# Kernel optimization log

Measured on AMD Instinct MI355X. Metric: run time of the kernel, lower is better.

Reference implementation:

```python
import jax, jax.numpy as jnp
import numpy as np

HEADS = 4
LN_EPS = 1e-5

def layernorm(x, w, b):
    m = x.mean(-1, keepdims=True)
    v = ((x - m) ** 2).mean(-1, keepdims=True)
    return (x - m) * jax.lax.rsqrt(v + LN_EPS) * w + b

def conv3d(x, w, b, pad, dil=1, groups=1):
    out = jax.lax.conv_general_dilated(
        x, w, (1, 1, 1), [(pad, pad)] * 3,
        rhs_dilation=(dil, dil, dil),
        dimension_numbers=('NCDHW', 'OIDHW', 'NCDHW'),
        feature_group_count=groups)
    return out + b[None, :, None, None, None]

def trilinear_gather(x_flat, pz, py, px, D, H, W):
    # x_flat: [B,C,S]; pz/py/px: [B,S] fractional sample coords, zero padding outside
    z0f, y0f, x0f = jnp.floor(pz), jnp.floor(py), jnp.floor(px)
    wz, wy, wx = pz - z0f, py - y0f, px - x0f
    z0, y0, x0 = z0f.astype(jnp.int32), y0f.astype(jnp.int32), x0f.astype(jnp.int32)
    acc = jnp.zeros_like(x_flat)
    for dz in (0, 1):
        for dy in (0, 1):
            for dx in (0, 1):
                iz, iy, ix = z0 + dz, y0 + dy, x0 + dx
                cw = (wz if dz else 1.0 - wz) * (wy if dy else 1.0 - wy) * (wx if dx else 1.0 - wx)
                valid = (iz >= 0) & (iz < D) & (iy >= 0) & (iy < H) & (ix >= 0) & (ix < W)
                idx = (jnp.clip(iz, 0, D - 1) * H + jnp.clip(iy, 0, H - 1)) * W + jnp.clip(ix, 0, W - 1)
                vals = jnp.take_along_axis(x_flat, idx[:, None, :], axis=2)
                acc = acc + vals * (cw * valid)[:, None, :]
    return acc

def deform_conv3d(x, off_w, off_b, w, b):
    # DeformConvPack: offsets from a regular 3x3x3 conv, then offset trilinear sampling + conv
    B, C, D, H, W = x.shape
    K = 27
    offsets = conv3d(x, off_w, off_b, 1).reshape(B, K, 3, D * H * W)
    gz, gy, gx = jnp.indices((D, H, W))
    bz = gz.reshape(-1).astype(x.dtype)[None]
    by = gy.reshape(-1).astype(x.dtype)[None]
    bx = gx.reshape(-1).astype(x.dtype)[None]
    x_flat = x.reshape(B, C, -1)
    O = w.shape[0]
    wk = w.reshape(O, C, K)
    out = jnp.zeros((B, O, D * H * W), x.dtype)
    for k in range(K):  # fixed 27 kernel taps
        kz, ky, kx = k // 9, (k // 3) % 3, k % 3
        pz = bz + (kz - 1) + offsets[:, k, 0]
        py = by + (ky - 1) + offsets[:, k, 1]
        px = bx + (kx - 1) + offsets[:, k, 2]
        samp = trilinear_gather(x_flat, pz, py, px, D, H, W)  # [B,C,S]
        out = out + jnp.einsum('bcs,oc->bos', samp, wk[:, :, k])
    out = out + b[None, :, None]
    return out.reshape(B, O, D, H, W)

def forward(x, temperature, qkv_w, norm_w, norm_b, proj1_w, proj1_b, conv0_w, conv0_b,
            convsp_w, convsp_b, off_w, off_b, dcn_w, dcn_b, conv1_w, conv1_b,
            proj2_w, proj2_b, norm2_w, norm2_b, out_w, out_b, H, W, D):
    B, N, C = x.shape
    hd = C // HEADS
    qkv = (x @ qkv_w.T).reshape(B, N, 3, HEADS, hd).transpose(2, 0, 3, 1, 4)  # [3,B,h,N,hd]
    q = qkv[0].transpose(0, 1, 3, 2)  # [B,h,hd,N]
    k = qkv[1].transpose(0, 1, 3, 2)
    v = qkv[2].transpose(0, 1, 3, 2)
    q = q / jnp.maximum(jnp.sqrt((q * q).sum(-1, keepdims=True)), 1e-12)
    k = k / jnp.maximum(jnp.sqrt((k * k).sum(-1, keepdims=True)), 1e-12)
    attn = jnp.einsum('bhcn,bhdn->bhcd', q, k) * temperature[None]
    attn = jax.nn.softmax(attn, axis=-1)
    x_ca = jnp.einsum('bhcd,bhdn->bhcn', attn, v).transpose(0, 3, 1, 2).reshape(B, N, C)
    x_ca = layernorm(x_ca, norm_w, norm_b)
    x5 = x_ca.transpose(0, 2, 1).reshape(B, C, H, W, D)
    shortcut = x5
    y = jnp.einsum('bcxyz,oc->boxyz', x5, proj1_w) + proj1_b[None, :, None, None, None]
    y = jax.nn.gelu(y, approximate=False)
    u = y
    a = conv3d(y, conv0_w, conv0_b, 2, 1, C)      # depthwise k=5 pad=2
    a = conv3d(a, convsp_w, convsp_b, 9, 3, C)    # depthwise k=7 pad=9 dil=3
    a = deform_conv3d(a, off_w, off_b, dcn_w, dcn_b)
    a = jnp.einsum('bcxyz,oc->boxyz', a, conv1_w) + conv1_b[None, :, None, None, None]
    y = u * a
    y = jnp.einsum('bcxyz,oc->boxyz', y, proj2_w) + proj2_b[None, :, None, None, None]
    y = y + shortcut
    x_sa = y.reshape(B, C, N).transpose(0, 2, 1)           # lka returns [B,N,C]
    x_sa = x_sa.reshape(B, C, N).transpose(0, 2, 1)        # faithful torch reshape-after-permute
    x_sa = layernorm(x_sa, norm2_w, norm2_b)
    return x_sa @ out_w.T + out_b

def setup_inputs():
    key = jax.random.key(0)
    ks = jax.random.split(key, 12)
    B, C, H, W, D = 2, 64, 32, 32, 32
    N = H * W * D
    s = 0.02
    return dict(
        x=jax.random.normal(ks[0], (B, N, C), jnp.float32),
        temperature=jnp.ones((HEADS, 1, 1), jnp.float32),
        qkv_w=jax.random.normal(ks[1], (3 * C, C), jnp.float32) * s,
        norm_w=jnp.ones((C,), jnp.float32), norm_b=jnp.zeros((C,), jnp.float32),
        proj1_w=jax.random.normal(ks[2], (C, C), jnp.float32) * s,
        proj1_b=jnp.zeros((C,), jnp.float32),
        conv0_w=jax.random.normal(ks[3], (C, 1, 5, 5, 5), jnp.float32) * s,
        conv0_b=jnp.zeros((C,), jnp.float32),
        convsp_w=jax.random.normal(ks[4], (C, 1, 7, 7, 7), jnp.float32) * s,
        convsp_b=jnp.zeros((C,), jnp.float32),
        off_w=jax.random.normal(ks[5], (81, C, 3, 3, 3), jnp.float32) * 0.01,
        off_b=jnp.zeros((81,), jnp.float32),
        dcn_w=jax.random.normal(ks[6], (C, C, 3, 3, 3), jnp.float32) * s,
        dcn_b=jnp.zeros((C,), jnp.float32),
        conv1_w=jax.random.normal(ks[7], (C, C), jnp.float32) * s,
        conv1_b=jnp.zeros((C,), jnp.float32),
        proj2_w=jax.random.normal(ks[8], (C, C), jnp.float32) * s,
        proj2_b=jnp.zeros((C,), jnp.float32),
        norm2_w=jnp.ones((C,), jnp.float32), norm2_b=jnp.zeros((C,), jnp.float32),
        out_w=jax.random.normal(ks[9], (C, C), jnp.float32) * s,
        out_b=jnp.zeros((C,), jnp.float32),
        B_in=B, C_in=C, H=H, W=W, D=D,
    )

def reference(x, temperature, qkv_w, norm_w, norm_b, proj1_w, proj1_b, conv0_w, conv0_b,
              convsp_w, convsp_b, off_w, off_b, dcn_w, dcn_b, conv1_w, conv1_b,
              proj2_w, proj2_b, norm2_w, norm2_b, out_w, out_b, B_in, C_in, H, W, D):
    return forward(x, temperature, qkv_w, norm_w, norm_b, proj1_w, proj1_b, conv0_w, conv0_b,
                   convsp_w, convsp_b, off_w, off_b, dcn_w, dcn_b, conv1_w, conv1_b,
                   proj2_w, proj2_b, norm2_w, norm2_b, out_w, out_b, H, W, D)
```

## Files before the change

### kernel.cpp

```cpp
#include <hip/hip_runtime.h>
#include <hip/hip_bf16.h>

#define S 32768
#define BUFN (2*64*32768)

typedef __bf16 v8bf __attribute__((ext_vector_type(8)));
typedef float v4f __attribute__((ext_vector_type(4)));
typedef int v4i __attribute__((ext_vector_type(4)));

__device__ __forceinline__ ushort f2b(float f) {
  union { float f; unsigned u; } v; v.f = f;
  unsigned r = (v.u + 0x7fffu + ((v.u >> 16) & 1u)) >> 16;
  return (ushort)r;
}
__device__ __forceinline__ float b2f(ushort h) {
  union { unsigned u; float f; } v; v.u = ((unsigned)h) << 16;
  return v.f;
}
__device__ __forceinline__ float u2f(unsigned u) {
  union { unsigned u; float f; } v; v.u = u;
  return v.f;
}

__global__ void k_wt(const float* __restrict__ offw, const float* __restrict__ dcnw,
                     ushort* __restrict__ wt_off16, ushort* __restrict__ wt_dcn16) {
  int i = blockIdx.x*256 + threadIdx.x;
  if (i < 27*96*64) {
    int c = i & 63, o = (i >> 6) % 96, t = i / 6144;
    wt_off16[i] = (o < 81) ? f2b(offw[o*1728 + c*27 + t]) : (ushort)0;
  }
  if (i < 27*64*64) {
    int c = i & 63, o = (i >> 6) & 63, k = i >> 12;
    wt_dcn16[i] = f2b(dcnw[(o*64 + c)*27 + k]);
  }
}

__global__ __launch_bounds__(256) void k_qkv(const float* __restrict__ x,
    const float* __restrict__ qkv_w, float* __restrict__ q,
    float* __restrict__ k, float* __restrict__ v) {
  __shared__ float wsm[96*64];
  int half = blockIdx.x >> 8;
  int gid  = ((blockIdx.x & 255) << 8) + threadIdx.x;
  int rbase = half * 96;
  for (int i = threadIdx.x; i < 96*64; i += 256) wsm[i] = qkv_w[rbase*64 + i];
  __syncthreads();
  int b = gid >> 15, n = gid & (S-1);
  const float* xr = x + (size_t)gid * 64;
  float xv[64];
#pragma unroll
  for (int i = 0; i < 16; i++) {
    float4 t = ((const float4*)xr)[i];
    xv[4*i]=t.x; xv[4*i+1]=t.y; xv[4*i+2]=t.z; xv[4*i+3]=t.w;
  }
  for (int r = 0; r < 96; r++) {
    const float4* wr4 = (const float4*)&wsm[r*64];
    float acc = 0.f;
#pragma unroll
    for (int c4 = 0; c4 < 16; c4++) {
      float4 wv4 = wr4[c4];
      acc += xv[4*c4]*wv4.x + xv[4*c4+1]*wv4.y + xv[4*c4+2]*wv4.z + xv[4*c4+3]*wv4.w;
    }
    int row = rbase + r;
    float* dst = (row < 64) ? q : (row < 128 ? k : v);
    int ch = row & 63;
    dst[((size_t)(b*64 + ch))*S + n] = acc;
  }
}

__global__ __launch_bounds__(256) void k_rownorm(const float* __restrict__ q,
    const float* __restrict__ k, float* __restrict__ inv) {
  int row = blockIdx.x;
  const float* p = (row < 128) ? (q + (size_t)row*S) : (k + (size_t)(row-128)*S);
  const float4* p4 = (const float4*)p;
  float ss = 0.f;
  for (int i = threadIdx.x; i < S/4; i += 256) {
    float4 t = p4[i];
    ss += t.x*t.x + t.y*t.y + t.z*t.z + t.w*t.w;
  }
  __shared__ float red[256];
  red[threadIdx.x] = ss; __syncthreads();
  for (int st = 128; st > 0; st >>= 1) {
    if (threadIdx.x < st) red[threadIdx.x] += red[threadIdx.x+st];
    __syncthreads();
  }
  if (threadIdx.x == 0) inv[row] = 1.0f / fmaxf(sqrtf(red[0]), 1e-12f);
}

__global__ __launch_bounds__(256) void k_gram(const float* __restrict__ q,
    const float* __restrict__ k, float* __restrict__ gram) {
  __shared__ float qt[16][65], kt[16][65];
  int bi = blockIdx.x;
  int b = bi >> 7, h = (bi >> 5) & 3, chunk = bi & 31;
  int c = threadIdx.x >> 4, d = threadIdx.x & 15;
  const float* qb = q + ((size_t)(b*64 + h*16))*S;
  const float* kb = k + ((size_t)(b*64 + h*16))*S;
  int lr = threadIdx.x >> 4, lc = (threadIdx.x & 15) * 4;
  float acc = 0.f;
  for (int n0 = chunk*1024; n0 < chunk*1024 + 1024; n0 += 64) {
    float4 tq = *(const float4*)(qb + (size_t)lr*S + n0 + lc);
    float4 tk = *(const float4*)(kb + (size_t)lr*S + n0 + lc);
    __syncthreads();
    qt[lr][lc]=tq.x; qt[lr][lc+1]=tq.y; qt[lr][lc+2]=tq.z; qt[lr][lc+3]=tq.w;
    kt[lr][lc]=tk.x; kt[lr][lc+1]=tk.y; kt[lr][lc+2]=tk.z; kt[lr][lc+3]=tk.w;
    __syncthreads();
#pragma unroll
    for (int nn = 0; nn < 64; nn++) acc += qt[c][nn]*kt[d][nn];
  }
  atomicAdd(&gram[((b*4+h)*16+c)*16 + d], acc);
}

__global__ __launch_bounds__(256) void k_xca_ln(const float* __restrict__ v,
    const float* __restrict__ gram, const float* __restrict__ inv,
    const float* __restrict__ temp,
    const float* __restrict__ nw, const float* __restrict__ nb,
    float* __restrict__ x5) {
  __shared__ float at[1024];
  __shared__ float wsh[64], bsh[64];
  int gid = blockIdx.x*256 + threadIdx.x;
  int b = gid >> 15, n = gid & (S-1);
  int tid = threadIdx.x;
  if (tid < 64) {
    int h = tid >> 4, c = tid & 15;
    float iq = inv[b*64 + h*16 + c];
    float tp = temp[h];
    float l[16], m = -1e30f;
#pragma unroll
    for (int d = 0; d < 16; d++) {
      float vv = gram[((b*4+h)*16+c)*16 + d] * iq * inv[128 + b*64 + h*16 + d] * tp;
      l[d] = vv; m = fmaxf(m, vv);
    }
    float s = 0.f;
#pragma unroll
    for (int d = 0; d < 16; d++) { l[d] = expf(l[d]-m); s += l[d]; }
    float is = 1.0f / s;
#pragma unroll
    for (int d = 0; d < 16; d++) at[(h*16+c)*16 + d] = l[d]*is;
  } else if (tid < 128) {
    wsh[tid-64] = nw[tid-64]; bsh[tid-64] = nb[tid-64];
  }
  __syncthreads();
  const float* vb = v + (size_t)b*64*S + n;
  float vv[64];
#pragma unroll
  for (int ch = 0; ch < 64; ch++) vv[ch] = vb[(size_t)ch*S];
  float xc[64];
#pragma unroll
  for (int h = 0; h < 4; h++)
#pragma unroll
    for (int cc = 0; cc < 16; cc++) {
      float a = 0.f;
#pragma unroll
      for (int d = 0; d < 16; d++) a += at[(h*16+cc)*16 + d] * vv[h*16+d];
      xc[h*16+cc] = a;
    }
  float mean = 0.f;
#pragma unroll
  for (int ch = 0; ch < 64; ch++) mean += xc[ch];
  mean *= (1.0f/64.0f);
  float var = 0.f;
#pragma unroll
  for (int ch = 0; ch < 64; ch++) { float d = xc[ch]-mean; var += d*d; }
  var *= (1.0f/64.0f);
  float rs = rsqrtf(var + 1e-5f);
  float* xb = x5 + (size_t)b*64*S + n;
#pragma unroll
  for (int ch = 0; ch < 64; ch++)
    xb[(size_t)ch*S] = (xc[ch]-mean)*rs*wsh[ch] + bsh[ch];
}

__global__ __launch_bounds__(256) void k_proj1(const float* __restrict__ x5,
    const float* __restrict__ w, const float* __restrict__ bias, float* __restrict__ u) {
  __shared__ float wsm[32*64];
  __shared__ float bsm[32];
  int half = blockIdx.x >> 8;
  int gid = ((blockIdx.x & 255) << 8) + threadIdx.x;
  int o0 = half*32;
  for (int i = threadIdx.x; i < 32*64; i += 256) wsm[i] = w[o0*64 + i];
  if (threadIdx.x < 32) bsm[threadIdx.x] = bias[o0 + threadIdx.x];
  __syncthreads();
  int b = gid >> 15, n = gid & (S-1);
  const float* xb = x5 + (size_t)b*64*S + n;
  float xv[64];
#pragma unroll
  for (int ch = 0; ch < 64; ch++) xv[ch] = xb[(size_t)ch*S];
  float* ub = u + (size_t)b*64*S + n;
  for (int oo = 0; oo < 32; oo++) {
    const float4* wr4 = (const float4*)&wsm[oo*64];
    float acc = bsm[oo];
#pragma unroll
    for (int c4 = 0; c4 < 16; c4++) {
      float4 wv4 = wr4[c4];
      acc += xv[4*c4]*wv4.x + xv[4*c4+1]*wv4.y + xv[4*c4+2]*wv4.z + xv[4*c4+3]*wv4.w;
    }
    float g = 0.5f*acc*(1.0f + erff(acc*0.70710678118654752f));
    ub[(size_t)(o0+oo)*S] = g;
  }
}

__global__ __launch_bounds__(256) void k_conv0(const float* __restrict__ in,
    const float* __restrict__ w, const float* __restrict__ bias, ushort* __restrict__ out) {
  __shared__ ushort tile[5*32*40];
  __shared__ float wsh[128];
  int bi = blockIdx.x;
  int z = bi & 31, c = (bi >> 5) & 63, b = bi >> 11;
  const float* ib = in + ((size_t)(b*64+c) << 15);
  for (int i = threadIdx.x; i < 800; i += 256)
    ((int4*)tile)[i] = make_int4(0,0,0,0);
  if (threadIdx.x < 125) wsh[threadIdx.x] = w[c*125 + threadIdx.x];
  __syncthreads();
  for (int i = threadIdx.x; i < 5*1024; i += 256) {
    int dz = i >> 10, r = i & 1023;
    int zg = z + dz - 2;
    if (zg >= 0 && zg < 32)
      tile[(dz*32 + (r >> 5))*40 + (r & 31) + 2] = f2b(ib[zg*1024 + r]);
  }
  __syncthreads();
  int y = threadIdx.x >> 3, x0 = (threadIdx.x & 7) << 2;
  float bv = bias[c];
  float acc[4] = {bv, bv, bv, bv};
  for (int dz = 0; dz < 5; dz++) {
#pragma unroll
    for (int dy = 0; dy < 5; dy++) {
      int yy = y + dy - 2;
      if (yy < 0 || yy >= 32) continue;
      const float* wp = &wsh[(dz*5+dy)*5];
      float wreg[5];
#pragma unroll
      for (int dx = 0; dx < 5; dx++) wreg[dx] = wp[dx];
      const ushort* rp = &tile[(dz*32+yy)*40 + x0];
      int2 rl = *(const int2*)rp;
      int2 rh = *(const int2*)(rp + 4);
      float row[8];
      row[0]=u2f(((unsigned)rl.x)<<16); row[1]=u2f(rl.x & 0xffff0000u);
      row[2]=u2f(((unsigned)rl.y)<<16); row[3]=u2f(rl.y & 0xffff0000u);
      row[4]=u2f(((unsigned)rh.x)<<16); row[5]=u2f(rh.x & 0xffff0000u);
      row[6]=u2f(((unsigned)rh.y)<<16); row[7]=u2f(rh.y & 0xffff0000u);
#pragma unroll
      for (int dx = 0; dx < 5; dx++)
#pragma unroll
        for (int j = 0; j < 4; j++)
          acc[j] += wreg[dx] * row[dx+j];
    }
  }
  ushort* ob = out + ((size_t)(b*64+c) << 15) + z*1024 + y*32 + x0;
  unsigned p0 = (unsigned)f2b(acc[0]) | ((unsigned)f2b(acc[1]) << 16);
  unsigned p1 = (unsigned)f2b(acc[2]) | ((unsigned)f2b(acc[3]) << 16);
  *(int2*)ob = make_int2((int)p0, (int)p1);
}

__global__ __launch_bounds__(256) void k_convsp(const ushort* __restrict__ in,
    const float* __restrict__ w, const float* __restrict__ bias, ushort* __restrict__ out) {
  __shared__ ushort tile[7*32*56];
  __shared__ float wsh[344];
  int bi = blockIdx.x;
  int z = bi & 31, c = (bi >> 5) & 63, b = bi >> 11;
  const ushort* ib = in + ((size_t)(b*64+c) << 15);
  for (int i = threadIdx.x; i < 1568; i += 256)
    ((int4*)tile)[i] = make_int4(0,0,0,0);
  for (int i = threadIdx.x; i < 343; i += 256) wsh[i] = w[c*343 + i];
  __syncthreads();
  for (int i = threadIdx.x; i < 7*1024; i += 256) {
    int t = i >> 10, r = i & 1023;
    int zg = z + 3*t - 9;
    if (zg >= 0 && zg < 32)
      tile[(t*32 + (r >> 5))*56 + (r & 31) + 9] = ib[zg*1024 + r];
  }
  __syncthreads();
  int y = threadIdx.x >> 3, x0 = (threadIdx.x & 7) << 2;
  float bv = bias[c];
  float acc[4] = {bv, bv, bv, bv};
  for (int t = 0; t < 7; t++) {
#pragma unroll
    for (int dy = 0; dy < 7; dy++) {
      int yy = y + 3*dy - 9;
      if (yy < 0 || yy >= 32) continue;
      const float* wp = &wsh[(t*7+dy)*7];
      float wreg[7];
#pragma unroll
      for (int dx = 0; dx < 7; dx++) wreg[dx] = wp[dx];
      const ushort* rp = &tile[(t*32+yy)*56 + x0];
      float row[24];
#pragma unroll
      for (int qq = 0; qq < 6; qq++) {
        int2 rv = *(const int2*)(rp + 4*qq);
        row[4*qq+0]=u2f(((unsigned)rv.x)<<16); row[4*qq+1]=u2f(rv.x & 0xffff0000u);
        row[4*qq+2]=u2f(((unsigned)rv.y)<<16); row[4*qq+3]=u2f(rv.y & 0xffff0000u);
      }
#pragma unroll
      for (int dx = 0; dx < 7; dx++)
#pragma unroll
        for (int j = 0; j < 4; j++)
          acc[j] += wreg[dx] * row[3*dx+j];
    }
  }
  ushort* ob = out + ((size_t)(b*64+c) << 15) + z*1024 + y*32 + x0;
  unsigned p0 = (unsigned)f2b(acc[0]) | ((unsigned)f2b(acc[1]) << 16);
  unsigned p1 = (unsigned)f2b(acc[2]) | ((unsigned)f2b(acc[3]) << 16);
  *(int2*)ob = make_int2((int)p0, (int)p1);
}

__global__ __launch_bounds__(256) void k_tr(const ushort* __restrict__ a2,
                                            ushort* __restrict__ a2t) {
  __shared__ ushort tile[64*66];
  int bi = blockIdx.x;
  int b = bi >> 9, chunk = bi & 511;
  int s0 = chunk << 6;
  const ushort* ib = a2 + ((size_t)b << 21) + s0;
#pragma unroll
  for (int i = 0; i < 16; i++) {
    int j = threadIdx.x + (i << 8);
    int c = j >> 6, sl = j & 63;
    tile[c*66 + sl] = ib[((size_t)c << 15) + sl];
  }
  __syncthreads();
  ushort* ob = a2t + ((size_t)b << 21) + ((size_t)s0 << 6);
#pragma unroll
  for (int i = 0; i < 16; i++) {
    int j = threadIdx.x + (i << 8);
    int sl = j >> 6, c = j & 63;
    ob[sl*64 + c] = tile[c*66 + sl];
  }
}

__global__ __launch_bounds__(256) void k_offconv(const ushort* __restrict__ a2t,
    const ushort* __restrict__ wt16, float* __restrict__ off) {
  int bi = blockIdx.x;
  int b = bi >> 9, tile = bi & 511;
  int s0 = tile << 6;
  int tid = threadIdx.x;
  int lane = tid & 63, wv = tid >> 6;
  int si = lane & 15, rq = lane >> 4, q8 = rq << 3;
  int sw = s0 + (wv << 4);
  int s_c = sw + si;
  int zc = s_c >> 10, yc = (s_c >> 5) & 31, xc = s_c & 31;
  const ushort* a2b = a2t + ((size_t)b << 21);
  v4f acc[6];
#pragma unroll
  for (int i = 0; i < 6; i++) acc[i] = (v4f){0.f,0.f,0.f,0.f};
  const v4i z4 = {0,0,0,0};
  for (int t = 0; t < 27; t++) {
    int kz = t/9, ky = (t/3)%3, kx = t%3;
    int zz = zc + kz - 1, yy = yc + ky - 1, xx = xc + kx - 1;
    bool ok = (zz>=0 && zz<32 && yy>=0 && yy<32 && xx>=0 && xx<32);
    v8bf b0 = __builtin_bit_cast(v8bf, z4);
    v8bf b1 = __builtin_bit_cast(v8bf, z4);
    if (ok) {
      const ushort* p = a2b + ((size_t)((zz<<10)+(yy<<5)+xx) << 6) + q8;
      b0 = *(const v8bf*)p;
      b1 = *(const v8bf*)(p + 32);
    }
    const ushort* wk = wt16 + t*6144;
#pragma unroll
    for (int ot = 0; ot < 6; ot++) {
      const ushort* ap = wk + (((ot<<4) + si) << 6) + q8;
      v8bf a0 = *(const v8bf*)ap;
      v8bf a1 = *(const v8bf*)(ap + 32);
      acc[ot] = __builtin_amdgcn_mfma_f32_16x16x32_bf16(a0, b0, acc[ot], 0,0,0);
      acc[ot] = __builtin_amdgcn_mfma_f32_16x16x32_bf16(a1, b1, acc[ot], 0,0,0);
    }
  }
#pragma unroll
  for (int ot = 0; ot < 6; ot++)
#pragma unroll
    for (int r = 0; r < 4; r++) {
      int o = ot*16 + rq*4 + r;
      if (o < 81)
        off[(((size_t)(b*81 + o)) << 15) + sw + si] = acc[ot][r];
    }
}

__global__ __launch_bounds__(256) void k_dcn(const ushort* __restrict__ a2t,
    const float* __restrict__ off, const float* __restrict__ off_b,
    const ushort* __restrict__ wt16, float* __restrict__ out) {
  __shared__ float ofs[81*66];
  __shared__ ushort scr[4][16*72];
  int bi = blockIdx.x;
  int b = bi >> 9, tile = bi & 511;
  int s0 = tile << 6;
  int tid = threadIdx.x;
  const float* offbase = off + (((size_t)(b*81)) << 15) + s0;
  for (int i = tid; i < 5184; i += 256) {
    int r = i >> 6, sl = i & 63;
    ofs[r*66 + sl] = offbase[((size_t)r << 15) + sl] + off_b[r];
  }
  __syncthreads();
  int lane = tid & 63, wv = tid >> 6;
  int sr = lane >> 3, cs = lane & 7;
  int si = lane & 15, rq = lane >> 4;
  int sw = s0 + (wv << 4);
  const ushort* a2b = a2t + ((size_t)b << 21);
  ushort* myscr = &scr[wv][0];
  int sA = sw + sr, sB = sw + 8 + sr;
  int zA = sA >> 10, yA = (sA >> 5) & 31, xA = sA & 31;
  int zB = sB >> 10, yB = (sB >> 5) & 31, xB = sB & 31;
  int slcA = (wv << 4) + sr, slcB = slcA + 8;
  v4f acc[4];
#pragma unroll
  for (int t = 0; t < 4; t++) acc[t] = (v4f){0.f,0.f,0.f,0.f};
  for (int k = 0; k < 27; k++) {
    int kz = k/9, ky = (k/3)%3, kx = k%3;
    int idxA[8], idxB[8];
    float wA[8], wB[8];
    {
      float pz = (float)(zA + kz - 1) + ofs[(3*k+0)*66 + slcA];
      float py = (float)(yA + ky - 1) + ofs[(3*k+1)*66 + slcA];
      float px = (float)(xA + kx - 1) + ofs[(3*k+2)*66 + slcA];
      float fz = floorf(pz), fy = floorf(py), fx = floorf(px);
      float wz = pz-fz, wy = py-fy, wx = px-fx;
      int z0 = (int)fz, y0 = (int)fy, x0 = (int)fx;
      int zi[2], yi[2], xi[2]; float zw[2], yw[2], xw[2];
#pragma unroll
      for (int d = 0; d < 2; d++) {
        int iz = z0 + d; zi[d] = min(max(iz,0),31) << 10;
        zw[d] = (iz >= 0 && iz < 32) ? (d ? wz : 1.f-wz) : 0.f;
        int iy = y0 + d; yi[d] = min(max(iy,0),31) << 5;
        yw[d] = (iy >= 0 && iy < 32) ? (d ? wy : 1.f-wy) : 0.f;
        int ix = x0 + d; xi[d] = min(max(ix,0),31);
        xw[d] = (ix >= 0 && ix < 32) ? (d ? wx : 1.f-wx) : 0.f;
      }
#pragma unroll
      for (int r = 0; r < 8; r++) {
        int dz = r >> 2, dy = (r >> 1) & 1, dx = r & 1;
        idxA[r] = zi[dz] + yi[dy] + xi[dx];
        wA[r] = zw[dz] * yw[dy] * xw[dx];
      }
    }
    {
      float pz = (float)(zB + kz - 1) + ofs[(3*k+0)*66 + slcB];
      float py = (float)(yB + ky - 1) + ofs[(3*k+1)*66 + slcB];
      float px = (float)(xB + kx - 1) + ofs[(3*k+2)*66 + slcB];
      float fz = floorf(pz), fy = floorf(py), fx = floorf(px);
      float wz = pz-fz, wy = py-fy, wx = px-fx;
      int z0 = (int)fz, y0 = (int)fy, x0 = (int)fx;
      int zi[2], yi[2], xi[2]; float zw[2], yw[2], xw[2];
#pragma unroll
      for (int d = 0; d < 2; d++) {
        int iz = z0 + d; zi[d] = min(max(iz,0),31) << 10;
        zw[d] = (iz >= 0 && iz < 32) ? (d ? wz : 1.f-wz) : 0.f;
        int iy = y0 + d; yi[d] = min(max(iy,0),31) << 5;
        yw[d] = (iy >= 0 && iy < 32) ? (d ? wy : 1.f-wy) : 0.f;
        int ix = x0 + d; xi[d] = min(max(ix,0),31);
        xw[d] = (ix >= 0 && ix < 32) ? (d ? wx : 1.f-wx) : 0.f;
      }
#pragma unroll
      for (int r = 0; r < 8; r++) {
        int dz = r >> 2, dy = (r >> 1) & 1, dx = r & 1;
        idxB[r] = zi[dz] + yi[dy] + xi[dx];
        wB[r] = zw[dz] * yw[dy] * xw[dx];
      }
    }
    v4i gA[8], gB[8];
#pragma unroll
    for (int r = 0; r < 8; r++)
      gA[r] = *(const v4i*)(a2b + ((size_t)idxA[r] << 6) + (cs << 3));
#pragma unroll
    for (int r = 0; r < 8; r++)
      gB[r] = *(const v4i*)(a2b + ((size_t)idxB[r] << 6) + (cs << 3));
    float faA[8], faB[8];
#pragma unroll
    for (int j = 0; j < 8; j++) { faA[j] = 0.f; faB[j] = 0.f; }
#pragma unroll
    for (int r = 0; r < 8; r++) {
      float wa = wA[r], wb = wB[r];
#pragma unroll
      for (int m = 0; m < 4; m++) {
        unsigned da = (unsigned)gA[r][m];
        faA[2*m]   += wa * u2f(da << 16);
        faA[2*m+1] += wa * u2f(da & 0xffff0000u);
        unsigned db = (unsigned)gB[r][m];
        faB[2*m]   += wb * u2f(db << 16);
        faB[2*m+1] += wb * u2f(db & 0xffff0000u);
      }
    }
    v4i dA, dB;
#pragma unroll
    for (int m = 0; m < 4; m++) {
      unsigned l0 = (__float_as_uint(faA[2*m])   + 0x8000u) >> 16;
      unsigned h0 = (__float_as_uint(faA[2*m+1]) + 0x8000u) & 0xffff0000u;
      dA[m] = (int)(l0 | h0);
      unsigned l1 = (__float_as_uint(faB[2*m])   + 0x8000u) >> 16;
      unsigned h1 = (__float_as_uint(faB[2*m+1]) + 0x8000u) & 0xffff0000u;
      dB[m] = (int)(l1 | h1);
    }
    *(v4i*)&myscr[sr*72 + (cs << 3)]       = dA;
    *(v4i*)&myscr[(8+sr)*72 + (cs << 3)]   = dB;
    v8bf bf0 = *(const v8bf*)&myscr[si*72 + (rq << 3)];
    v8bf bf1 = *(const v8bf*)&myscr[si*72 + 32 + (rq << 3)];
    const ushort* wk = wt16 + (k << 12);
#pragma unroll
    for (int ot = 0; ot < 4; ot++) {
      const ushort* ap = wk + (((ot<<4) + si) << 6) + (rq << 3);
      v8bf a0 = *(const v8bf*)ap;
      v8bf a1 = *(const v8bf*)(ap + 32);
      acc[ot] = __builtin_amdgcn_mfma_f32_16x16x32_bf16(a0, bf0, acc[ot], 0,0,0);
      acc[ot] = __builtin_amdgcn_mfma_f32_16x16x32_bf16(a1, bf1, acc[ot], 0,0,0);
    }
  }
#pragma unroll
  for (int ot = 0; ot < 4; ot++)
#pragma unroll
    for (int r = 0; r < 4; r++) {
      int o = (ot << 4) + rq*4 + r;
      out[(((size_t)(b*64 + o)) << 15) + sw + si] = acc[ot][r];
    }
}

__global__ __launch_bounds__(256) void k_fuse2(const float* __restrict__ dcn0,
    const float* __restrict__ dcn_b, const float* __restrict__ c1w,
    const float* __restrict__ c1b, const float* __restrict__ u,
    const float* __restrict__ p2w, const float* __restrict__ p2b,
    const float* __restrict__ x5, float* __restrict__ y2) {
  __shared__ float w1[4096], w2[4096];
  __shared__ float b1[64], b2[64], db[64];
  int gid = blockIdx.x*256 + threadIdx.x;
  for (int i = threadIdx.x; i < 4096; i += 256) { w1[i] = c1w[i]; w2[i] = p2w[i]; }
  if (threadIdx.x < 64) {
    b1[threadIdx.x]=c1b[threadIdx.x]; b2[threadIdx.x]=p2b[threadIdx.x];
    db[threadIdx.x]=dcn_b[threadIdx.x];
  }
  __syncthreads();
  int b = gid >> 15, n = gid & (S-1);
  const float* dbp0 = dcn0 + (size_t)b*64*S + n;
  float dv[64];
#pragma unroll
  for (int c = 0; c < 64; c++)
    dv[c] = dbp0[(size_t)c*S] + db[c];
  const float* ub = u + (size_t)b*64*S + n;
  float m[64];
  for (int o = 0; o < 64; o++) {
    const float4* w4 = (const float4*)&w1[o*64];
    float a = b1[o];
#pragma unroll
    for (int c4 = 0; c4 < 16; c4++) {
      float4 wv4 = w4[c4];
      a += dv[4*c4]*wv4.x + dv[4*c4+1]*wv4.y + dv[4*c4+2]*wv4.z + dv[4*c4+3]*wv4.w;
    }
    m[o] = ub[(size_t)o*S] * a;
  }
  const float* sb = x5 + (size_t)b*64*S + n;
  float* yb = y2 + (size_t)b*64*S + n;
  for (int o = 0; o < 64; o++) {
    const float4* w4 = (const float4*)&w2[o*64];
    float a = b2[o];
#pragma unroll
    for (int c4 = 0; c4 < 16; c4++) {
      float4 wv4 = w4[c4];
      a += m[4*c4]*wv4.x + m[4*c4+1]*wv4.y + m[4*c4+2]*wv4.z + m[4*c4+3]*wv4.w;
    }
    yb[(size_t)o*S] = a + sb[(size_t)o*S];
  }
}

__global__ __launch_bounds__(256) void k_final(const float* __restrict__ y2,
    const float* __restrict__ n2w, const float* __restrict__ n2b,
    const float* __restrict__ ow, const float* __restrict__ ob, float* __restrict__ out) {
  __shared__ float wsh[4096];
  __shared__ float nw[64], nb[64], obs[64];
  int bi = blockIdx.x;
  int b = bi >> 7; int mg = (bi >> 4) & 7; int r0 = (bi & 15)*4;
  for (int i = threadIdx.x; i < 4096; i += 256) wsh[i] = ow[i];
  if (threadIdx.x < 64) {
    nw[threadIdx.x]=n2w[threadIdx.x]; nb[threadIdx.x]=n2b[threadIdx.x];
    obs[threadIdx.x]=ob[threadIdx.x];
  }
  __syncthreads();
  int mi = threadIdx.x & 63, rg = threadIdx.x >> 6;
  int r = r0 + rg;
  int m = mg*64 + mi;
  int n = m*64 + r;
  const float* yb = y2 + ((size_t)(b*64+r))*S + m;
  float v[64];
#pragma unroll
  for (int c = 0; c < 64; c++) v[c] = yb[(size_t)c*512];
  float mean = 0.f;
#pragma unroll
  for (int c = 0; c < 64; c++) mean += v[c];
  mean *= (1.0f/64.0f);
  float var = 0.f;
#pragma unroll
  for (int c = 0; c < 64; c++) { float d = v[c]-mean; var += d*d; }
  var *= (1.0f/64.0f);
  float rs = rsqrtf(var + 1e-5f);
#pragma unroll
  for (int c = 0; c < 64; c++) v[c] = (v[c]-mean)*rs*nw[c] + nb[c];
  float* orow = out + ((size_t)b*S + n)*64;
  for (int o4 = 0; o4 < 16; o4++) {
    const float4* w0 = (const float4*)&wsh[(o4*4+0)*64];
    const float4* w1 = (const float4*)&wsh[(o4*4+1)*64];
    const float4* w2 = (const float4*)&wsh[(o4*4+2)*64];
    const float4* w3 = (const float4*)&wsh[(o4*4+3)*64];
    float t0=obs[o4*4+0], t1=obs[o4*4+1], t2=obs[o4*4+2], t3=obs[o4*4+3];
#pragma unroll
    for (int c4 = 0; c4 < 16; c4++) {
      float4 a0 = w0[c4], a1 = w1[c4], a2 = w2[c4], a3 = w3[c4];
      float v0 = v[4*c4], v1 = v[4*c4+1], v2 = v[4*c4+2], v3 = v[4*c4+3];
      t0 += a0.x*v0 + a0.y*v1 + a0.z*v2 + a0.w*v3;
      t1 += a1.x*v0 + a1.y*v1 + a1.z*v2 + a1.w*v3;
      t2 += a2.x*v0 + a2.y*v1 + a2.z*v2 + a2.w*v3;
      t3 += a3.x*v0 + a3.y*v1 + a3.z*v2 + a3.w*v3;
    }
    float4 a; a.x=t0; a.y=t1; a.z=t2; a.w=t3;
    ((float4*)orow)[o4] = a;
  }
}

extern "C" void kernel_launch(void* const* d_in, const int* in_sizes, int n_in,
                              void* d_out, int out_size, void* d_ws, size_t ws_size,
                              hipStream_t stream) {
  const float* x      = (const float*)d_in[0];
  const float* temp   = (const float*)d_in[1];
  const float* qkv_w  = (const float*)d_in[2];
  const float* norm_w = (const float*)d_in[3];
  const float* norm_b = (const float*)d_in[4];
  const float* p1w    = (const float*)d_in[5];
  const float* p1b    = (const float*)d_in[6];
  const float* c0w    = (const float*)d_in[7];
  const float* c0b    = (const float*)d_in[8];
  const float* cspw   = (const float*)d_in[9];
  const float* cspb   = (const float*)d_in[10];
  const float* offw   = (const float*)d_in[11];
  const float* offb   = (const float*)d_in[12];
  const float* dcnw   = (const float*)d_in[13];
  const float* dcnb   = (const float*)d_in[14];
  const float* c1w    = (const float*)d_in[15];
  const float* c1b    = (const float*)d_in[16];
  const float* p2w    = (const float*)d_in[17];
  const float* p2b    = (const float*)d_in[18];
  const float* n2w    = (const float*)d_in[19];
  const float* n2b    = (const float*)d_in[20];
  const float* outw   = (const float*)d_in[21];
  const float* outb   = (const float*)d_in[22];
  float* out = (float*)d_out;

  float* Wa  = (float*)d_ws;
  float* Wb  = Wa + BUFN;
  float* Wc  = Wb + BUFN;
  float* OFF = Wc + BUFN;
  float* SM  = OFF + (size_t)2*81*S;
  float* SM_inv  = SM;
  float* SM_gram = SM + 256;
  ushort* WT_OFF16 = (ushort*)(SM + 4352);
  ushort* WT_DCN16 = WT_OFF16 + 165888;
  float* vbuf = out;
  ushort* A1_16 = (ushort*)d_out;
  ushort* A2_16 = (ushort*)Wc;
  ushort* a2t = (ushort*)d_out;

  hipMemsetAsync(SM, 0, 4352*sizeof(float), stream);
  k_wt     <<<648, 256, 0, stream>>>(offw, dcnw, WT_OFF16, WT_DCN16);

  k_qkv    <<<512, 256, 0, stream>>>(x, qkv_w, Wa, Wb, vbuf);
  k_rownorm<<<256, 256, 0, stream>>>(Wa, Wb, SM_inv);
  k_gram   <<<256, 256, 0, stream>>>(Wa, Wb, SM_gram);
  k_xca_ln <<<256, 256, 0, stream>>>(vbuf, SM_gram, SM_inv, temp, norm_w, norm_b, Wa);
  k_proj1  <<<512, 256, 0, stream>>>(Wa, p1w, p1b, Wb);
  k_conv0  <<<4096,256, 0, stream>>>(Wb, c0w, c0b, A1_16);
  k_convsp <<<4096,256, 0, stream>>>(A1_16, cspw, cspb, A2_16);
  k_tr     <<<1024,256, 0, stream>>>(A2_16, a2t);
  k_offconv<<<1024,256, 0, stream>>>(a2t, WT_OFF16, OFF);
  k_dcn    <<<1024,256, 0, stream>>>(a2t, OFF, offb, WT_DCN16, Wc);
  k_fuse2  <<<256, 256, 0, stream>>>(Wc, dcnb, c1w, c1b, Wb, p2w, p2b, Wa, OFF);
  k_final  <<<256, 256, 0, stream>>>(OFF, n2w, n2b, outw, outb, out);
}
```

Baseline: 833.7 us.

## Use bf16 MFMA for QKV and proj1 pointwise projections

Rewrites the QKV and proj1 1x1 projections to use 16x16x32 bf16 MFMA instructions instead of scalar fp32 FMA loops. Weights are pre-converted to bf16 in the weight-prep kernel, and activations are converted to bf16 in registers before the matrix ops. This is meant to cut the ALU-bound per-thread dot products and the LDS weight staging, at the cost of bf16 rounding of inputs and weights in these two projections.

```diff
diff --git a/kernel.cpp b/kernel.cpp
--- a/kernel.cpp
+++ b/kernel.cpp
@@ -23,7 +23,9 @@
 }
 
 __global__ void k_wt(const float* __restrict__ offw, const float* __restrict__ dcnw,
-                     ushort* __restrict__ wt_off16, ushort* __restrict__ wt_dcn16) {
+                     const float* __restrict__ qkvw, const float* __restrict__ p1w,
+                     ushort* __restrict__ wt_off16, ushort* __restrict__ wt_dcn16,
+                     ushort* __restrict__ qkv16, ushort* __restrict__ p1w16) {
   int i = blockIdx.x*256 + threadIdx.x;
   if (i < 27*96*64) {
     int c = i & 63, o = (i >> 6) % 96, t = i / 6144;
@@ -33,37 +35,54 @@
     int c = i & 63, o = (i >> 6) & 63, k = i >> 12;
     wt_dcn16[i] = f2b(dcnw[(o*64 + c)*27 + k]);
   }
+  if (i < 12288) qkv16[i] = f2b(qkvw[i]);
+  if (i < 4096)  p1w16[i] = f2b(p1w[i]);
 }
 
 __global__ __launch_bounds__(256) void k_qkv(const float* __restrict__ x,
-    const float* __restrict__ qkv_w, float* __restrict__ q,
+    const ushort* __restrict__ qkvw16, float* __restrict__ q,
     float* __restrict__ k, float* __restrict__ v) {
-  __shared__ float wsm[96*64];
-  int half = blockIdx.x >> 8;
-  int gid  = ((blockIdx.x & 255) << 8) + threadIdx.x;
-  int rbase = half * 96;
-  for (int i = threadIdx.x; i < 96*64; i += 256) wsm[i] = qkv_w[rbase*64 + i];
-  __syncthreads();
-  int b = gid >> 15, n = gid & (S-1);
-  const float* xr = x + (size_t)gid * 64;
-  float xv[64];
-#pragma unroll
-  for (int i = 0; i < 16; i++) {
-    float4 t = ((const float4*)xr)[i];
-    xv[4*i]=t.x; xv[4*i+1]=t.y; xv[4*i+2]=t.z; xv[4*i+3]=t.w;
-  }
-  for (int r = 0; r < 96; r++) {
-    const float4* wr4 = (const float4*)&wsm[r*64];
-    float acc = 0.f;
-#pragma unroll
-    for (int c4 = 0; c4 < 16; c4++) {
-      float4 wv4 = wr4[c4];
-      acc += xv[4*c4]*wv4.x + xv[4*c4+1]*wv4.y + xv[4*c4+2]*wv4.z + xv[4*c4+3]*wv4.w;
-    }
-    int row = rbase + r;
-    float* dst = (row < 64) ? q : (row < 128 ? k : v);
-    int ch = row & 63;
-    dst[((size_t)(b*64 + ch))*S + n] = acc;
+  int bi = blockIdx.x;
+  int b = bi >> 9, tile = bi & 511;
+  int tid = threadIdx.x;
+  int lane = tid & 63, wv = tid >> 6;
+  int si = lane & 15, rq = lane >> 4, q8 = rq << 3;
+  int s = (tile << 6) + (wv << 4) + si;
+  const float* xr = x + ((size_t)(b*S + s) << 6);
+  float4 t0 = *(const float4*)(xr + q8);
+  float4 t1 = *(const float4*)(xr + q8 + 4);
+  float4 t2 = *(const float4*)(xr + q8 + 32);
+  float4 t3 = *(const float4*)(xr + q8 + 36);
+  float f0[8] = {t0.x,t0.y,t0.z,t0.w,t1.x,t1.y,t1.z,t1.w};
+  float f1[8] = {t2.x,t2.y,t2.z,t2.w,t3.x,t3.y,t3.z,t3.w};
+  v4i d0, d1;
+#pragma unroll
+  for (int m = 0; m < 4; m++) {
+    d0[m] = (int)((unsigned)f2b(f0[2*m]) | ((unsigned)f2b(f0[2*m+1]) << 16));
+    d1[m] = (int)((unsigned)f2b(f1[2*m]) | ((unsigned)f2b(f1[2*m+1]) << 16));
+  }
+  v8bf b0 = __builtin_bit_cast(v8bf, d0);
+  v8bf b1 = __builtin_bit_cast(v8bf, d1);
+  v4f acc[12];
+#pragma unroll
+  for (int t = 0; t < 12; t++) acc[t] = (v4f){0.f,0.f,0.f,0.f};
+#pragma unroll
+  for (int t = 0; t < 12; t++) {
+    const ushort* ap = qkvw16 + (((t<<4) + si) << 6) + q8;
+    v8bf a0 = *(const v8bf*)ap;
+    v8bf a1 = *(const v8bf*)(ap + 32);
+    acc[t] = __builtin_amdgcn_mfma_f32_16x16x32_bf16(a0, b0, acc[t], 0,0,0);
+    acc[t] = __builtin_amdgcn_mfma_f32_16x16x32_bf16(a1, b1, acc[t], 0,0,0);
+  }
+#pragma unroll
+  for (int t = 0; t < 12; t++) {
+    float* dst = (t < 4) ? q : (t < 8 ? k : v);
+    int chb = (t & 3) << 4;
+#pragma unroll
+    for (int r = 0; r < 4; r++) {
+      int ch = chb + rq*4 + r;
+      dst[((size_t)(b*64 + ch))*S + s] = acc[t][r];
+    }
   }
 }
 
@@ -169,32 +188,49 @@
 }
 
 __global__ __launch_bounds__(256) void k_proj1(const float* __restrict__ x5,
-    const float* __restrict__ w, const float* __restrict__ bias, float* __restrict__ u) {
-  __shared__ float wsm[32*64];
-  __shared__ float bsm[32];
-  int half = blockIdx.x >> 8;
-  int gid = ((blockIdx.x & 255) << 8) + threadIdx.x;
-  int o0 = half*32;
-  for (int i = threadIdx.x; i < 32*64; i += 256) wsm[i] = w[o0*64 + i];
-  if (threadIdx.x < 32) bsm[threadIdx.x] = bias[o0 + threadIdx.x];
-  __syncthreads();
-  int b = gid >> 15, n = gid & (S-1);
-  const float* xb = x5 + (size_t)b*64*S + n;
-  float xv[64];
-#pragma unroll
-  for (int ch = 0; ch < 64; ch++) xv[ch] = xb[(size_t)ch*S];
-  float* ub = u + (size_t)b*64*S + n;
-  for (int oo = 0; oo < 32; oo++) {
-    const float4* wr4 = (const float4*)&wsm[oo*64];
-    float acc = bsm[oo];
-#pragma unroll
-    for (int c4 = 0; c4 < 16; c4++) {
-      float4 wv4 = wr4[c4];
-      acc += xv[4*c4]*wv4.x + xv[4*c4+1]*wv4.y + xv[4*c4+2]*wv4.z + xv[4*c4+3]*wv4.w;
-    }
-    float g = 0.5f*acc*(1.0f + erff(acc*0.70710678118654752f));
-    ub[(size_t)(o0+oo)*S] = g;
-  }
+    const ushort* __restrict__ p1w16, const float* __restrict__ bias, float* __restrict__ u) {
+  int bi = blockIdx.x;
+  int b = bi >> 9, tile = bi & 511;
+  int tid = threadIdx.x;
+  int lane = tid & 63, wv = tid >> 6;
+  int si = lane & 15, rq = lane >> 4, q8 = rq << 3;
+  int s = (tile << 6) + (wv << 4) + si;
+  const float* xb = x5 + ((size_t)b << 21) + s;
+  float f0[8], f1[8];
+#pragma unroll
+  for (int j = 0; j < 8; j++) {
+    f0[j] = xb[(size_t)(q8 + j) << 15];
+    f1[j] = xb[(size_t)(32 + q8 + j) << 15];
+  }
+  v4i d0, d1;
+#pragma unroll
+  for (int m = 0; m < 4; m++) {
+    d0[m] = (int)((unsigned)f2b(f0[2*m]) | ((unsigned)f2b(f0[2*m+1]) << 16));
+    d1[m] = (int)((unsigned)f2b(f1[2*m]) | ((unsigned)f2b(f1[2*m+1]) << 16));
+  }
+  v8bf b0 = __builtin_bit_cast(v8bf, d0);
+  v8bf b1 = __builtin_bit_cast(v8bf, d1);
+  v4f acc[4];
+#pragma unroll
+  for (int t = 0; t < 4; t++) acc[t] = (v4f){0.f,0.f,0.f,0.f};
+#pragma unroll
+  for (int t = 0; t < 4; t++) {
+    const ushort* ap = p1w16 + (((t<<4) + si) << 6) + q8;
+    v8bf a0 = *(const v8bf*)ap;
+    v8bf a1 = *(const v8bf*)(ap + 32);
+    acc[t] = __builtin_amdgcn_mfma_f32_16x16x32_bf16(a0, b0, acc[t], 0,0,0);
+    acc[t] = __builtin_amdgcn_mfma_f32_16x16x32_bf16(a1, b1, acc[t], 0,0,0);
+  }
+  float* ub = u + ((size_t)b << 21) + s;
+#pragma unroll
+  for (int t = 0; t < 4; t++)
+#pragma unroll
+    for (int r = 0; r < 4; r++) {
+      int ch = (t << 4) + rq*4 + r;
+      float a = acc[t][r] + bias[ch];
+      float g = 0.5f*a*(1.0f + erff(a*0.70710678118654752f));
+      ub[(size_t)ch << 15] = g;
+    }
 }
 
 __global__ __launch_bounds__(256) void k_conv0(const float* __restrict__ in,
@@ -641,19 +677,21 @@
   float* SM_gram = SM + 256;
   ushort* WT_OFF16 = (ushort*)(SM + 4352);
   ushort* WT_DCN16 = WT_OFF16 + 165888;
+  ushort* QKV16    = WT_DCN16 + 110592;
+  ushort* P1W16    = QKV16 + 12288;
   float* vbuf = out;
   ushort* A1_16 = (ushort*)d_out;
   ushort* A2_16 = (ushort*)Wc;
   ushort* a2t = (ushort*)d_out;
 
   hipMemsetAsync(SM, 0, 4352*sizeof(float), stream);
-  k_wt     <<<648, 256, 0, stream>>>(offw, dcnw, WT_OFF16, WT_DCN16);
-
-  k_qkv    <<<512, 256, 0, stream>>>(x, qkv_w, Wa, Wb, vbuf);
+  k_wt     <<<648, 256, 0, stream>>>(offw, dcnw, qkv_w, p1w, WT_OFF16, WT_DCN16, QKV16, P1W16);
+
+  k_qkv    <<<1024,256, 0, stream>>>(x, QKV16, Wa, Wb, vbuf);
   k_rownorm<<<256, 256, 0, stream>>>(Wa, Wb, SM_inv);
   k_gram   <<<256, 256, 0, stream>>>(Wa, Wb, SM_gram);
   k_xca_ln <<<256, 256, 0, stream>>>(vbuf, SM_gram, SM_inv, temp, norm_w, norm_b, Wa);
-  k_proj1  <<<512, 256, 0, stream>>>(Wa, p1w, p1b, Wb);
+  k_proj1  <<<1024,256, 0, stream>>>(Wa, P1W16, p1b, Wb);
   k_conv0  <<<4096,256, 0, stream>>>(Wb, c0w, c0b, A1_16);
   k_convsp <<<4096,256, 0, stream>>>(A1_16, cspw, cspb, A2_16);
   k_tr     <<<1024,256, 0, stream>>>(A2_16, a2t);
```

New measurement: 791.7 us. 1.05x faster.
